# Kernel tuning notes

Measured on AMD Instinct MI355X. Metric: run time of the kernel, lower is better.

## Reference

```python
import jax, jax.numpy as jnp
import numpy as np

N_NODES = 50000
N_EDGES = 800000
N_GRAPHS = 128
IN_F = 768
NHID = 64
HID2 = NHID * 2  # 128
N_CLS = 2


def setup_inputs() -> dict:
    key = jax.random.key(0)
    ks = jax.random.split(key, 16)
    s = lambda k, shp, fan: jax.random.normal(k, shp, jnp.float32) / np.sqrt(fan)
    return {
        "x": jax.random.normal(ks[0], (N_NODES, IN_F), jnp.float32),
        "edge_index": jax.random.randint(ks[1], (2, N_EDGES), 0, N_NODES, jnp.int64),
        "batch": jnp.sort(jax.random.randint(ks[2], (N_NODES,), 0, N_GRAPHS, jnp.int64)),
        "W1": s(ks[3], (IN_F, HID2), IN_F),
        "as1": s(ks[4], (HID2,), HID2),
        "ad1": s(ks[5], (HID2,), HID2),
        "b1": jnp.zeros((HID2,), jnp.float32),
        "W2": s(ks[6], (HID2, HID2), HID2),
        "as2": s(ks[7], (HID2,), HID2),
        "ad2": s(ks[8], (HID2,), HID2),
        "b2": jnp.zeros((HID2,), jnp.float32),
        "fc1_w": s(ks[9], (HID2, NHID), HID2),
        "fc1_b": jnp.zeros((NHID,), jnp.float32),
        "fc2_w": s(ks[10], (NHID, N_CLS), NHID),
        "fc2_b": jnp.zeros((N_CLS,), jnp.float32),
    }


def _gat_conv(x, W, a_src, a_dst, b, src, dst):
    # PyG GATConv, heads=1, self-loops already included in (src, dst).
    xw = x @ W                                   # [N, F_out]
    e_src = xw @ a_src                           # [N]
    e_dst = xw @ a_dst                           # [N]
    e = jax.nn.leaky_relu(e_src[src] + e_dst[dst], 0.2)   # [E]
    m = jax.ops.segment_max(e, dst, num_segments=N_NODES)  # per-dst max (stable softmax)
    num = jnp.exp(e - m[dst])
    den = jax.ops.segment_sum(num, dst, num_segments=N_NODES)
    alpha = num / den[dst]                       # [E]
    out = jax.ops.segment_sum(alpha[:, None] * xw[src], dst, num_segments=N_NODES)
    return out + b


def reference(x, edge_index, batch, W1, as1, ad1, b1, W2, as2, ad2, b2,
              fc1_w, fc1_b, fc2_w, fc2_b):
    # add self loops (PyG GATConv default add_self_loops=True)
    loops = jnp.arange(N_NODES, dtype=edge_index.dtype)
    src = jnp.concatenate([edge_index[0], loops])
    dst = jnp.concatenate([edge_index[1], loops])

    h = jax.nn.selu(_gat_conv(x, W1, as1, ad1, b1, src, dst))
    h = jax.nn.selu(_gat_conv(h, W2, as2, ad2, b2, src, dst))

    # global mean pool over graphs
    sums = jax.ops.segment_sum(h, batch, num_segments=N_GRAPHS)          # [G, HID2]
    cnts = jax.ops.segment_sum(jnp.ones((N_NODES,), h.dtype), batch, num_segments=N_GRAPHS)
    pooled = jax.nn.selu(sums / jnp.maximum(cnts, 1.0)[:, None])

    g = jax.nn.selu(pooled @ fc1_w + fc1_b)      # dropout is identity in eval mode
    logits = g @ fc2_w + fc2_b
    return jax.nn.log_softmax(logits, axis=-1)
```

## Files before the change

### kernel.cpp

```cpp
#include <hip/hip_runtime.h>
#include <math.h>

#define N_NODES  50000
#define N_EDGES  800000
#define E_TOT    (N_EDGES + N_NODES)
#define N_GRAPHS 128
#define IN_F     768
#define HID2     128
#define NHID     64

typedef __attribute__((ext_vector_type(8))) short bf16x8;
typedef __attribute__((ext_vector_type(4))) float f32x4;
typedef __attribute__((ext_vector_type(4))) unsigned short us4;

__device__ __forceinline__ float selu_f(float x) {
    const float alpha = 1.6732632423543772f;
    const float scale = 1.0507009873554805f;
    return scale * (x > 0.f ? x : alpha * (expf(x) - 1.f));
}

__device__ __forceinline__ unsigned short f2bf(float f) {
    unsigned u = __float_as_uint(f);
    u += 0x7FFFu + ((u >> 16) & 1u);
    return (unsigned short)(u >> 16);
}

__global__ void setup_k(const float* __restrict__ W1, const float* __restrict__ W2,
                        unsigned short* __restrict__ Wt1, unsigned short* __restrict__ Wt2,
                        unsigned* __restrict__ deg) {
    int i = blockIdx.x * blockDim.x + threadIdx.x;
    if (i < N_NODES) deg[i] = 0u;
    if (i < 128 * IN_F) {
        int n = i / IN_F, k = i - n * IN_F;
        Wt1[i] = f2bf(W1[(long)k * 128 + n]);
    }
    if (i < 128 * HID2) {
        int n = i >> 7, k = i & 127;
        Wt2[i] = f2bf(W2[(long)k * 128 + n]);
    }
}

#define LDA2 72
__global__ __launch_bounds__(256) void gemm_mfma(
        const float* __restrict__ A, const unsigned short* __restrict__ Bt,
        float* __restrict__ C, int M, int K) {
    __shared__ unsigned short As[64 * LDA2];
    __shared__ unsigned short Bs[128 * LDA2];
    const int tid  = threadIdx.x;
    const int row0 = blockIdx.x * 64;
    const int w    = tid >> 6;
    const int lane = tid & 63;
    const int quad = lane >> 4;
    const int l16  = lane & 15;
    const int m_off = (w & 1) * 32;
    const int n_off = (w >> 1) * 64;

    f32x4 acc[2][4];
#pragma unroll
    for (int mi = 0; mi < 2; mi++)
#pragma unroll
        for (int ni = 0; ni < 4; ni++)
            acc[mi][ni] = (f32x4){0.f, 0.f, 0.f, 0.f};

    float4 aR[4];
    bf16x8 bR[4];
#pragma unroll
    for (int i = 0; i < 4; i++) {
        int p = tid + i * 256;
        int r = p >> 4, c4 = p & 15;
        int gr = row0 + r;
        aR[i] = (gr < M) ? *(const float4*)&A[(long)gr * K + c4 * 4]
                         : make_float4(0.f, 0.f, 0.f, 0.f);
    }
#pragma unroll
    for (int i = 0; i < 4; i++) {
        int c = tid + i * 256;
        int n = c >> 3, koff = (c & 7) * 8;
        bR[i] = *(const bf16x8*)&Bt[(long)n * K + koff];
    }

    for (int k0 = 0; k0 < K; k0 += 64) {
#pragma unroll
        for (int i = 0; i < 4; i++) {
            int p = tid + i * 256;
            int r = p >> 4, c4 = p & 15;
            us4 o;
            o.x = f2bf(aR[i].x); o.y = f2bf(aR[i].y);
            o.z = f2bf(aR[i].z); o.w = f2bf(aR[i].w);
            *(us4*)&As[r * LDA2 + c4 * 4] = o;
        }
#pragma unroll
        for (int i = 0; i < 4; i++) {
            int c = tid + i * 256;
            int n = c >> 3, koff = (c & 7) * 8;
            *(bf16x8*)&Bs[n * LDA2 + koff] = bR[i];
        }
        __syncthreads();

        if (k0 + 64 < K) {
            int k1 = k0 + 64;
#pragma unroll
            for (int i = 0; i < 4; i++) {
                int p = tid + i * 256;
                int r = p >> 4, c4 = p & 15;
                int gr = row0 + r;
                aR[i] = (gr < M) ? *(const float4*)&A[(long)gr * K + k1 + c4 * 4]
                                 : make_float4(0.f, 0.f, 0.f, 0.f);
            }
#pragma unroll
            for (int i = 0; i < 4; i++) {
                int c = tid + i * 256;
                int n = c >> 3, koff = (c & 7) * 8;
                bR[i] = *(const bf16x8*)&Bt[(long)n * K + k1 + koff];
            }
        }

        bf16x8 af[2][2], bfr[2][4];
#pragma unroll
        for (int kk = 0; kk < 2; kk++) {
#pragma unroll
            for (int mi = 0; mi < 2; mi++)
                af[kk][mi] = *(const bf16x8*)&As[(m_off + mi * 16 + l16) * LDA2 + kk * 32 + quad * 8];
#pragma unroll
            for (int ni = 0; ni < 4; ni++)
                bfr[kk][ni] = *(const bf16x8*)&Bs[(n_off + ni * 16 + l16) * LDA2 + kk * 32 + quad * 8];
        }
#pragma unroll
        for (int kk = 0; kk < 2; kk++)
#pragma unroll
            for (int mi = 0; mi < 2; mi++)
#pragma unroll
                for (int ni = 0; ni < 4; ni++)
                    acc[mi][ni] = __builtin_amdgcn_mfma_f32_16x16x32_bf16(
                        af[kk][mi], bfr[kk][ni], acc[mi][ni], 0, 0, 0);
        __syncthreads();
    }

#pragma unroll
    for (int mi = 0; mi < 2; mi++)
#pragma unroll
        for (int r = 0; r < 4; r++) {
            int row = row0 + m_off + mi * 16 + quad * 4 + r;
            if (row < M) {
#pragma unroll
                for (int ni = 0; ni < 4; ni++)
                    C[(long)row * 128 + n_off + ni * 16 + l16] = acc[mi][ni][r];
            }
        }
}

__global__ void node_e(const float* __restrict__ xw,
                       const float* __restrict__ a_s, const float* __restrict__ a_d,
                       float* __restrict__ e_src, float* __restrict__ e_dst) {
    int i = blockIdx.x * blockDim.x + threadIdx.x;
    if (i >= N_NODES) return;
    const float4* row = (const float4*)(xw + (long)i * HID2);
    float s = 0.f, d = 0.f;
#pragma unroll
    for (int j = 0; j < 32; j++) {
        float4 v = row[j];
        float4 as = ((const float4*)a_s)[j];
        float4 ad = ((const float4*)a_d)[j];
        s += v.x * as.x + v.y * as.y + v.z * as.z + v.w * as.w;
        d += v.x * ad.x + v.y * ad.y + v.z * ad.z + v.w * ad.w;
    }
    e_src[i] = s;
    e_dst[i] = d;
}

__global__ void deg_hist(const int* __restrict__ ei, unsigned* __restrict__ deg) {
    int e = blockIdx.x * blockDim.x + threadIdx.x;
    if (e < N_EDGES) atomicAdd(&deg[ei[N_EDGES + e]], 1u);
}

__global__ __launch_bounds__(256) void scan_seed(const unsigned* __restrict__ deg,
                                                 unsigned* __restrict__ row_ptr,
                                                 unsigned* __restrict__ cursor,
                                                 unsigned* __restrict__ csr_src) {
    __shared__ unsigned psum_s[4];
    __shared__ unsigned wsum[4];
    int tid = threadIdx.x;
    int wid = tid >> 6, lane = tid & 63;
    int chunk0 = blockIdx.x * 256;

    unsigned psum = 0;
    for (int i = tid; i < chunk0; i += 256) psum += deg[i] + 1u;
    for (int o = 32; o; o >>= 1) psum += __shfl_xor(psum, o);
    if (lane == 0) psum_s[wid] = psum;

    int i = chunk0 + tid;
    unsigned v = (i < N_NODES) ? deg[i] + 1u : 0u;
    unsigned x = v;
    for (int o = 1; o < 64; o <<= 1) {
        unsigned y = __shfl_up(x, o);
        if (lane >= o) x += y;
    }
    if (lane == 63) wsum[wid] = x;
    __syncthreads();
    unsigned base = psum_s[0] + psum_s[1] + psum_s[2] + psum_s[3];
    unsigned wbase = 0;
    for (int k = 0; k < wid; k++) wbase += wsum[k];
    if (i < N_NODES) {
        unsigned rp = base + wbase + x - v;
        row_ptr[i] = rp;
        csr_src[rp] = (unsigned)i;
        cursor[i] = rp + 1;
        if (i == N_NODES - 1) row_ptr[N_NODES] = rp + v;
    }
}

__global__ void csr_scatter(const int* __restrict__ ei,
                            unsigned* __restrict__ cursor, unsigned* __restrict__ csr_src) {
    int e = blockIdx.x * blockDim.x + threadIdx.x;
    if (e >= N_EDGES) return;
    int d = ei[N_EDGES + e];
    unsigned p = atomicAdd(&cursor[d], 1u);
    csr_src[p] = (unsigned)ei[e];
}

__global__ __launch_bounds__(256) void gat_agg(
        const unsigned* __restrict__ row_ptr, const unsigned* __restrict__ csr_src,
        const float* __restrict__ e_src, const float* __restrict__ e_dst,
        const float* __restrict__ xw, const float* __restrict__ bias,
        float* __restrict__ out) {
    __shared__ float2 buf[4][64];
    int wv = threadIdx.x >> 6;
    int node = blockIdx.x * 4 + wv;
    if (node >= N_NODES) return;
    int lane = threadIdx.x & 63;
    unsigned beg = row_ptr[node], end = row_ptr[node + 1];
    int deg = (int)(end - beg);
    float ed = e_dst[node];

    float a0 = 0.f, a1 = 0.f, den = 0.f;
    for (int base = 0; base < deg; base += 64) {
        int i = base + lane;
        float num = 0.f;
        unsigned s = 0u;
        if (i < deg) {
            s = csr_src[beg + i];
            float e = e_src[s] + ed;
            e = e > 0.f ? e : 0.2f * e;
            num = __expf(e);
            den += num;
        }
        float2 pk; pk.x = num; pk.y = __uint_as_float(s);
        buf[wv][lane] = pk;

        int cnt = deg - base; if (cnt > 64) cnt = 64;
        int j = 0;
        for (; j + 4 <= cnt; j += 4) {
            float2 p0 = buf[wv][j + 0];
            float2 p1 = buf[wv][j + 1];
            float2 p2 = buf[wv][j + 2];
            float2 p3 = buf[wv][j + 3];
            float2 v0 = *(const float2*)&xw[(long)__float_as_uint(p0.y) * HID2 + lane * 2];
            float2 v1 = *(const float2*)&xw[(long)__float_as_uint(p1.y) * HID2 + lane * 2];
            float2 v2 = *(const float2*)&xw[(long)__float_as_uint(p2.y) * HID2 + lane * 2];
            float2 v3 = *(const float2*)&xw[(long)__float_as_uint(p3.y) * HID2 + lane * 2];
            a0 = fmaf(p0.x, v0.x, a0); a1 = fmaf(p0.x, v0.y, a1);
            a0 = fmaf(p1.x, v1.x, a0); a1 = fmaf(p1.x, v1.y, a1);
            a0 = fmaf(p2.x, v2.x, a0); a1 = fmaf(p2.x, v2.y, a1);
            a0 = fmaf(p3.x, v3.x, a0); a1 = fmaf(p3.x, v3.y, a1);
        }
        for (; j < cnt; j++) {
            float2 p = buf[wv][j];
            float2 v = *(const float2*)&xw[(long)__float_as_uint(p.y) * HID2 + lane * 2];
            a0 = fmaf(p.x, v.x, a0); a1 = fmaf(p.x, v.y, a1);
        }
    }
    for (int o = 32; o; o >>= 1) den += __shfl_xor(den, o);
    float inv = 1.f / den;
    out[(long)node * HID2 + lane * 2]     = selu_f(fmaf(a0, inv, bias[lane * 2]));
    out[(long)node * HID2 + lane * 2 + 1] = selu_f(fmaf(a1, inv, bias[lane * 2 + 1]));
}

__global__ __launch_bounds__(256) void pool_graph(
        const float* __restrict__ h, const int* __restrict__ batch,
        float* __restrict__ pooled) {
    int g = blockIdx.x;
    int lo = 0, hi = N_NODES;
    while (lo < hi) { int mid = (lo + hi) >> 1; if (batch[mid] < g) lo = mid + 1; else hi = mid; }
    int start = lo;
    lo = start; hi = N_NODES;
    while (lo < hi) { int mid = (lo + hi) >> 1; if (batch[mid] < g + 1) lo = mid + 1; else hi = mid; }
    int end = lo;

    int f = threadIdx.x & 127, half = threadIdx.x >> 7;
    float acc = 0.f;
    for (int n = start + half; n < end; n += 2) acc += h[(long)n * HID2 + f];
    __shared__ float part[HID2];
    if (half == 0) part[f] = acc;
    __syncthreads();
    if (half == 1) {
        float tot = part[f] + acc;
        float c = (float)(end - start);
        c = c > 1.f ? c : 1.f;
        pooled[g * HID2 + f] = selu_f(tot / c);
    }
}

__global__ void fc1_k(const float* __restrict__ pooled, const float* __restrict__ w,
                      const float* __restrict__ b, float* __restrict__ g) {
    __shared__ float row[HID2];
    int gi = blockIdx.x, j = threadIdx.x;
    row[j] = pooled[gi * HID2 + j];
    row[j + 64] = pooled[gi * HID2 + 64 + j];
    __syncthreads();
    float acc = b[j];
#pragma unroll
    for (int k = 0; k < HID2; k++) acc = fmaf(row[k], w[k * NHID + j], acc);
    g[gi * NHID + j] = selu_f(acc);
}

__global__ void fc2_k(const float* __restrict__ g, const float* __restrict__ w,
                      const float* __restrict__ b, float* __restrict__ out) {
    int gi = blockIdx.x * blockDim.x + threadIdx.x;
    if (gi >= N_GRAPHS) return;
    float l0 = b[0], l1 = b[1];
#pragma unroll
    for (int k = 0; k < NHID; k++) {
        float v = g[gi * NHID + k];
        l0 = fmaf(v, w[k * 2 + 0], l0);
        l1 = fmaf(v, w[k * 2 + 1], l1);
    }
    float m = fmaxf(l0, l1);
    float lse = m + logf(expf(l0 - m) + expf(l1 - m));
    out[gi * 2 + 0] = l0 - lse;
    out[gi * 2 + 1] = l1 - lse;
}

extern "C" void kernel_launch(void* const* d_in, const int* in_sizes, int n_in,
                              void* d_out, int out_size, void* d_ws, size_t ws_size,
                              hipStream_t stream) {
    const float* x     = (const float*)d_in[0];
    const int*   ei    = (const int*)d_in[1];
    const int*   batch = (const int*)d_in[2];
    const float* W1    = (const float*)d_in[3];
    const float* as1   = (const float*)d_in[4];
    const float* ad1   = (const float*)d_in[5];
    const float* b1    = (const float*)d_in[6];
    const float* W2    = (const float*)d_in[7];
    const float* as2   = (const float*)d_in[8];
    const float* ad2   = (const float*)d_in[9];
    const float* b2    = (const float*)d_in[10];
    const float* fc1w  = (const float*)d_in[11];
    const float* fc1b  = (const float*)d_in[12];
    const float* fc2w  = (const float*)d_in[13];
    const float* fc2b  = (const float*)d_in[14];
    float* out = (float*)d_out;

    float* ws = (float*)d_ws;
    const long NH = (long)N_NODES * HID2;
    float*    B0      = ws;
    float*    B1      = B0 + NH;
    float*    B2      = B1 + NH;
    float*    e_src   = B2 + NH;
    float*    e_dst   = e_src + N_NODES;
    unsigned* deg     = (unsigned*)(e_dst + N_NODES);
    unsigned* cursor  = deg + N_NODES;
    unsigned* row_ptr = cursor + N_NODES;
    unsigned* csr_src = row_ptr + N_NODES + 1;
    float*    pooled  = (float*)(csr_src + E_TOT);
    float*    g       = pooled + N_GRAPHS * HID2;
    unsigned short* Wt1 = (unsigned short*)(g + N_GRAPHS * NHID);
    unsigned short* Wt2 = Wt1 + 128 * IN_F;

    const int TB = 256;
    const int gNode = (N_NODES + TB - 1) / TB;
    const int gEdge = (N_EDGES + TB - 1) / TB;
    const int gGemm = (N_NODES + 63) / 64;
    const int gAgg  = (N_NODES + 3) / 4;

    setup_k<<<(128 * IN_F + TB - 1) / TB, TB, 0, stream>>>(W1, W2, Wt1, Wt2, deg);
    deg_hist<<<gEdge, TB, 0, stream>>>(ei, deg);
    scan_seed<<<gNode, TB, 0, stream>>>(deg, row_ptr, cursor, csr_src);
    csr_scatter<<<gEdge, TB, 0, stream>>>(ei, cursor, csr_src);

    gemm_mfma<<<gGemm, 256, 0, stream>>>(x, Wt1, B0, N_NODES, IN_F);
    node_e<<<gNode, TB, 0, stream>>>(B0, as1, ad1, e_src, e_dst);
    gat_agg<<<gAgg, 256, 0, stream>>>(row_ptr, csr_src, e_src, e_dst, B0, b1, B1);

    gemm_mfma<<<gGemm, 256, 0, stream>>>(B1, Wt2, B0, N_NODES, HID2);
    node_e<<<gNode, TB, 0, stream>>>(B0, as2, ad2, e_src, e_dst);
    gat_agg<<<gAgg, 256, 0, stream>>>(row_ptr, csr_src, e_src, e_dst, B0, b2, B2);

    pool_graph<<<N_GRAPHS, 256, 0, stream>>>(B2, batch, pooled);
    fc1_k<<<N_GRAPHS, NHID, 0, stream>>>(pooled, fc1w, fc1b, g);
    fc2_k<<<1, 128, 0, stream>>>(g, fc2w, fc2b, out);
}
```

Baseline: 591.4 us.

## Store intermediate node features in bf16 to halve gather traffic

The GEMM outputs (xw) and the first-layer aggregation output are now stored as bf16 instead of fp32. The node_e, gat_agg and second GEMM read them in bf16, which halves the bytes of the random neighbor gathers and of the intermediate writes and reads. The second GEMM also skips the fp32-to-bf16 conversion of its A operand. The cost is extra rounding of xw and h1 before the softmax-weighted aggregation and the attention logits, which may slightly change numerical accuracy.

```diff
diff --git a/kernel.cpp b/kernel.cpp
--- a/kernel.cpp
+++ b/kernel.cpp
@@ -23,6 +23,9 @@
     unsigned u = __float_as_uint(f);
     u += 0x7FFFu + ((u >> 16) & 1u);
     return (unsigned short)(u >> 16);
+}
+__device__ __forceinline__ float bf2f(unsigned short b) {
+    return __uint_as_float(((unsigned)b) << 16);
 }
 
 __global__ void setup_k(const float* __restrict__ W1, const float* __restrict__ W2,
@@ -41,11 +44,14 @@
 }
 
 #define LDA2 72
+template<bool ABF16, bool OUTBF16>
 __global__ __launch_bounds__(256) void gemm_mfma(
-        const float* __restrict__ A, const unsigned short* __restrict__ Bt,
-        float* __restrict__ C, int M, int K) {
+        const void* __restrict__ Av, const unsigned short* __restrict__ Bt,
+        void* __restrict__ Cv, int M, int K) {
     __shared__ unsigned short As[64 * LDA2];
     __shared__ unsigned short Bs[128 * LDA2];
+    const float* Af = (const float*)Av;
+    const unsigned short* Ab = (const unsigned short*)Av;
     const int tid  = threadIdx.x;
     const int row0 = blockIdx.x * 64;
     const int w    = tid >> 6;
@@ -63,14 +69,26 @@
             acc[mi][ni] = (f32x4){0.f, 0.f, 0.f, 0.f};
 
     float4 aR[4];
+    bf16x8 aRb[2];
     bf16x8 bR[4];
-#pragma unroll
-    for (int i = 0; i < 4; i++) {
-        int p = tid + i * 256;
-        int r = p >> 4, c4 = p & 15;
-        int gr = row0 + r;
-        aR[i] = (gr < M) ? *(const float4*)&A[(long)gr * K + c4 * 4]
-                         : make_float4(0.f, 0.f, 0.f, 0.f);
+    if (ABF16) {
+#pragma unroll
+        for (int i = 0; i < 2; i++) {
+            int p = tid + i * 256;
+            int r = p >> 3, c8 = p & 7;
+            int gr = row0 + r;
+            aRb[i] = (gr < M) ? *(const bf16x8*)&Ab[(long)gr * K + c8 * 8]
+                              : (bf16x8){0,0,0,0,0,0,0,0};
+        }
+    } else {
+#pragma unroll
+        for (int i = 0; i < 4; i++) {
+            int p = tid + i * 256;
+            int r = p >> 4, c4 = p & 15;
+            int gr = row0 + r;
+            aR[i] = (gr < M) ? *(const float4*)&Af[(long)gr * K + c4 * 4]
+                             : make_float4(0.f, 0.f, 0.f, 0.f);
+        }
     }
 #pragma unroll
     for (int i = 0; i < 4; i++) {
@@ -80,14 +98,23 @@
     }
 
     for (int k0 = 0; k0 < K; k0 += 64) {
-#pragma unroll
-        for (int i = 0; i < 4; i++) {
-            int p = tid + i * 256;
-            int r = p >> 4, c4 = p & 15;
-            us4 o;
-            o.x = f2bf(aR[i].x); o.y = f2bf(aR[i].y);
-            o.z = f2bf(aR[i].z); o.w = f2bf(aR[i].w);
-            *(us4*)&As[r * LDA2 + c4 * 4] = o;
+        if (ABF16) {
+#pragma unroll
+            for (int i = 0; i < 2; i++) {
+                int p = tid + i * 256;
+                int r = p >> 3, c8 = p & 7;
+                *(bf16x8*)&As[r * LDA2 + c8 * 8] = aRb[i];
+            }
+        } else {
+#pragma unroll
+            for (int i = 0; i < 4; i++) {
+                int p = tid + i * 256;
+                int r = p >> 4, c4 = p & 15;
+                us4 o;
+                o.x = f2bf(aR[i].x); o.y = f2bf(aR[i].y);
+                o.z = f2bf(aR[i].z); o.w = f2bf(aR[i].w);
+                *(us4*)&As[r * LDA2 + c4 * 4] = o;
+            }
         }
 #pragma unroll
         for (int i = 0; i < 4; i++) {
@@ -99,13 +126,24 @@
 
         if (k0 + 64 < K) {
             int k1 = k0 + 64;
-#pragma unroll
-            for (int i = 0; i < 4; i++) {
-                int p = tid + i * 256;
-                int r = p >> 4, c4 = p & 15;
-                int gr = row0 + r;
-                aR[i] = (gr < M) ? *(const float4*)&A[(long)gr * K + k1 + c4 * 4]
-                                 : make_float4(0.f, 0.f, 0.f, 0.f);
+            if (ABF16) {
+#pragma unroll
+                for (int i = 0; i < 2; i++) {
+                    int p = tid + i * 256;
+                    int r = p >> 3, c8 = p & 7;
+                    int gr = row0 + r;
+                    aRb[i] = (gr < M) ? *(const bf16x8*)&Ab[(long)gr * K + k1 + c8 * 8]
+                                      : (bf16x8){0,0,0,0,0,0,0,0};
+                }
+            } else {
+#pragma unroll
+                for (int i = 0; i < 4; i++) {
+                    int p = tid + i * 256;
+                    int r = p >> 4, c4 = p & 15;
+                    int gr = row0 + r;
+                    aR[i] = (gr < M) ? *(const float4*)&Af[(long)gr * K + k1 + c4 * 4]
+                                     : make_float4(0.f, 0.f, 0.f, 0.f);
+                }
             }
 #pragma unroll
             for (int i = 0; i < 4; i++) {
@@ -142,27 +180,37 @@
         for (int r = 0; r < 4; r++) {
             int row = row0 + m_off + mi * 16 + quad * 4 + r;
             if (row < M) {
-#pragma unroll
-                for (int ni = 0; ni < 4; ni++)
-                    C[(long)row * 128 + n_off + ni * 16 + l16] = acc[mi][ni][r];
+                if (OUTBF16) {
+                    unsigned short* C16 = (unsigned short*)Cv;
+#pragma unroll
+                    for (int ni = 0; ni < 4; ni++)
+                        C16[(long)row * 128 + n_off + ni * 16 + l16] = f2bf(acc[mi][ni][r]);
+                } else {
+                    float* Cf = (float*)Cv;
+#pragma unroll
+                    for (int ni = 0; ni < 4; ni++)
+                        Cf[(long)row * 128 + n_off + ni * 16 + l16] = acc[mi][ni][r];
+                }
             }
         }
 }
 
-__global__ void node_e(const float* __restrict__ xw,
+__global__ void node_e(const unsigned short* __restrict__ xw,
                        const float* __restrict__ a_s, const float* __restrict__ a_d,
                        float* __restrict__ e_src, float* __restrict__ e_dst) {
     int i = blockIdx.x * blockDim.x + threadIdx.x;
     if (i >= N_NODES) return;
-    const float4* row = (const float4*)(xw + (long)i * HID2);
+    const bf16x8* row = (const bf16x8*)(xw + (long)i * HID2);
     float s = 0.f, d = 0.f;
 #pragma unroll
-    for (int j = 0; j < 32; j++) {
-        float4 v = row[j];
-        float4 as = ((const float4*)a_s)[j];
-        float4 ad = ((const float4*)a_d)[j];
-        s += v.x * as.x + v.y * as.y + v.z * as.z + v.w * as.w;
-        d += v.x * ad.x + v.y * ad.y + v.z * ad.z + v.w * ad.w;
+    for (int j = 0; j < 16; j++) {
+        bf16x8 v = row[j];
+#pragma unroll
+        for (int e = 0; e < 8; e++) {
+            float f = bf2f((unsigned short)v[e]);
+            s = fmaf(f, a_s[j * 8 + e], s);
+            d = fmaf(f, a_d[j * 8 + e], d);
+        }
     }
     e_src[i] = s;
     e_dst[i] = d;
@@ -218,11 +266,12 @@
     csr_src[p] = (unsigned)ei[e];
 }
 
+template<bool OUTBF16>
 __global__ __launch_bounds__(256) void gat_agg(
         const unsigned* __restrict__ row_ptr, const unsigned* __restrict__ csr_src,
         const float* __restrict__ e_src, const float* __restrict__ e_dst,
-        const float* __restrict__ xw, const float* __restrict__ bias,
-        float* __restrict__ out) {
+        const unsigned short* __restrict__ xw, const float* __restrict__ bias,
+        void* __restrict__ outv) {
     __shared__ float2 buf[4][64];
     int wv = threadIdx.x >> 6;
     int node = blockIdx.x * 4 + wv;
@@ -254,25 +303,38 @@
             float2 p1 = buf[wv][j + 1];
             float2 p2 = buf[wv][j + 2];
             float2 p3 = buf[wv][j + 3];
-            float2 v0 = *(const float2*)&xw[(long)__float_as_uint(p0.y) * HID2 + lane * 2];
-            float2 v1 = *(const float2*)&xw[(long)__float_as_uint(p1.y) * HID2 + lane * 2];
-            float2 v2 = *(const float2*)&xw[(long)__float_as_uint(p2.y) * HID2 + lane * 2];
-            float2 v3 = *(const float2*)&xw[(long)__float_as_uint(p3.y) * HID2 + lane * 2];
-            a0 = fmaf(p0.x, v0.x, a0); a1 = fmaf(p0.x, v0.y, a1);
-            a0 = fmaf(p1.x, v1.x, a0); a1 = fmaf(p1.x, v1.y, a1);
-            a0 = fmaf(p2.x, v2.x, a0); a1 = fmaf(p2.x, v2.y, a1);
-            a0 = fmaf(p3.x, v3.x, a0); a1 = fmaf(p3.x, v3.y, a1);
+            unsigned q0 = *(const unsigned*)&xw[(long)__float_as_uint(p0.y) * HID2 + lane * 2];
+            unsigned q1 = *(const unsigned*)&xw[(long)__float_as_uint(p1.y) * HID2 + lane * 2];
+            unsigned q2 = *(const unsigned*)&xw[(long)__float_as_uint(p2.y) * HID2 + lane * 2];
+            unsigned q3 = *(const unsigned*)&xw[(long)__float_as_uint(p3.y) * HID2 + lane * 2];
+            a0 = fmaf(p0.x, __uint_as_float(q0 << 16), a0);
+            a1 = fmaf(p0.x, __uint_as_float(q0 & 0xffff0000u), a1);
+            a0 = fmaf(p1.x, __uint_as_float(q1 << 16), a0);
+            a1 = fmaf(p1.x, __uint_as_float(q1 & 0xffff0000u), a1);
+            a0 = fmaf(p2.x, __uint_as_float(q2 << 16), a0);
+            a1 = fmaf(p2.x, __uint_as_float(q2 & 0xffff0000u), a1);
+            a0 = fmaf(p3.x, __uint_as_float(q3 << 16), a0);
+            a1 = fmaf(p3.x, __uint_as_float(q3 & 0xffff0000u), a1);
         }
         for (; j < cnt; j++) {
             float2 p = buf[wv][j];
-            float2 v = *(const float2*)&xw[(long)__float_as_uint(p.y) * HID2 + lane * 2];
-            a0 = fmaf(p.x, v.x, a0); a1 = fmaf(p.x, v.y, a1);
+            unsigned q = *(const unsigned*)&xw[(long)__float_as_uint(p.y) * HID2 + lane * 2];
+            a0 = fmaf(p.x, __uint_as_float(q << 16), a0);
+            a1 = fmaf(p.x, __uint_as_float(q & 0xffff0000u), a1);
         }
     }
     for (int o = 32; o; o >>= 1) den += __shfl_xor(den, o);
     float inv = 1.f / den;
-    out[(long)node * HID2 + lane * 2]     = selu_f(fmaf(a0, inv, bias[lane * 2]));
-    out[(long)node * HID2 + lane * 2 + 1] = selu_f(fmaf(a1, inv, bias[lane * 2 + 1]));
+    float v0 = selu_f(fmaf(a0, inv, bias[lane * 2]));
+    float v1 = selu_f(fmaf(a1, inv, bias[lane * 2 + 1]));
+    if (OUTBF16) {
+        unsigned* ob = (unsigned*)outv;
+        ob[(long)node * 64 + lane] = ((unsigned)f2bf(v1) << 16) | (unsigned)f2bf(v0);
+    } else {
+        float* of = (float*)outv;
+        of[(long)node * HID2 + lane * 2]     = v0;
+        of[(long)node * HID2 + lane * 2 + 1] = v1;
+    }
 }
 
 __global__ __launch_bounds__(256) void pool_graph(
@@ -350,11 +412,10 @@
     const float* fc2b  = (const float*)d_in[14];
     float* out = (float*)d_out;
 
-    float* ws = (float*)d_ws;
     const long NH = (long)N_NODES * HID2;
-    float*    B0      = ws;
-    float*    B1      = B0 + NH;
-    float*    B2      = B1 + NH;
+    unsigned short* xwb = (unsigned short*)d_ws;
+    unsigned short* h1b = xwb + NH;
+    float*    B2      = (float*)(h1b + NH);
     float*    e_src   = B2 + NH;
     float*    e_dst   = e_src + N_NODES;
     unsigned* deg     = (unsigned*)(e_dst + N_NODES);
@@ -377,13 +438,13 @@
     scan_seed<<<gNode, TB, 0, stream>>>(deg, row_ptr, cursor, csr_src);
     csr_scatter<<<gEdge, TB, 0, stream>>>(ei, cursor, csr_src);
 
-    gemm_mfma<<<gGemm, 256, 0, stream>>>(x, Wt1, B0, N_NODES, IN_F);
-    node_e<<<gNode, TB, 0, stream>>>(B0, as1, ad1, e_src, e_dst);
-    gat_agg<<<gAgg, 256, 0, stream>>>(row_ptr, csr_src, e_src, e_dst, B0, b1, B1);
-
-    gemm_mfma<<<gGemm, 256, 0, stream>>>(B1, Wt2, B0, N_NODES, HID2);
-    node_e<<<gNode, TB, 0, stream>>>(B0, as2, ad2, e_src, e_dst);
-    gat_agg<<<gAgg, 256, 0, stream>>>(row_ptr, csr_src, e_src, e_dst, B0, b2, B2);
+    gemm_mfma<false, true><<<gGemm, 256, 0, stream>>>(x, Wt1, xwb, N_NODES, IN_F);
+    node_e<<<gNode, TB, 0, stream>>>(xwb, as1, ad1, e_src, e_dst);
+    gat_agg<true><<<gAgg, 256, 0, stream>>>(row_ptr, csr_src, e_src, e_dst, xwb, b1, h1b);
+
+    gemm_mfma<true, true><<<gGemm, 256, 0, stream>>>(h1b, Wt2, xwb, N_NODES, HID2);
+    node_e<<<gNode, TB, 0, stream>>>(xwb, as2, ad2, e_src, e_dst);
+    gat_agg<false><<<gAgg, 256, 0, stream>>>(row_ptr, csr_src, e_src, e_dst, xwb, b2, B2);
 
     pool_graph<<<N_GRAPHS, 256, 0, stream>>>(B2, batch, pooled);
     fc1_k<<<N_GRAPHS, NHID, 0, stream>>>(pooled, fc1w, fc1b, g);
```

Result: faster. 537.0 us (-9.2%).
